# Performance work log

Hardware: AMD Instinct MI355X
Metric: run time of the kernel (lower is better)

## Reference

```python
import jax, jax.numpy as jnp
import numpy as np

N_NODES = 50000
N_EDGES = 500000
D = 128  # in_size == out_size


def setup_inputs() -> dict:
    key = jax.random.key(0)
    ks = jax.random.split(key, 12)
    s = 1.0 / np.sqrt(D)
    feats = jax.random.normal(ks[0], (N_NODES, D), dtype=jnp.float32)
    # per-etype Linear params (torch Linear: y = x @ W.T + b)
    W_chem = jax.random.uniform(ks[1], (D, D), jnp.float32, -s, s)
    b_chem = jax.random.uniform(ks[2], (D,), jnp.float32, -s, s)
    W_elec = jax.random.uniform(ks[3], (D, D), jnp.float32, -s, s)
    b_elec = jax.random.uniform(ks[4], (D,), jnp.float32, -s, s)
    W_out = jax.random.uniform(ks[5], (D, D), jnp.float32, -s, s)
    b_out = jax.random.uniform(ks[6], (D,), jnp.float32, -s, s)
    src_chem = jax.random.randint(ks[7], (N_EDGES,), 0, N_NODES, dtype=jnp.int32)
    dst_chem = jax.random.randint(ks[8], (N_EDGES,), 0, N_NODES, dtype=jnp.int32)
    src_elec = jax.random.randint(ks[9], (N_EDGES,), 0, N_NODES, dtype=jnp.int32)
    dst_elec = jax.random.randint(ks[10], (N_EDGES,), 0, N_NODES, dtype=jnp.int32)
    return {
        "feats": feats,
        "W_chem": W_chem, "b_chem": b_chem,
        "W_elec": W_elec, "b_elec": b_elec,
        "W_out": W_out, "b_out": b_out,
        "src_chem": src_chem, "dst_chem": dst_chem,
        "src_elec": src_elec, "dst_elec": dst_elec,
    }


def reference(feats, W_chem, b_chem, W_elec, b_elec, W_out, b_out,
              src_chem, dst_chem, src_elec, dst_elec):
    n = feats.shape[0]
    # Per-etype linear projection of all node features
    Wh_chem = feats @ W_chem.T + b_chem  # [N, D]
    Wh_elec = feats @ W_elec.T + b_elec  # [N, D]
    # copy_src + sum scatter-aggregation per etype, merged with 'sum'
    h = jax.ops.segment_sum(Wh_chem[src_chem], dst_chem, num_segments=n)
    h = h + jax.ops.segment_sum(Wh_elec[src_elec], dst_elec, num_segments=n)
    # output Linear plus the last-iterated etype's Wh (quirk of original code:
    # 'electrical' is last in etypes order)
    return h @ W_out.T + b_out + Wh_elec
```

## Files before the change

kernel.cpp:

```cpp
#include <hip/hip_runtime.h>

#define D 128
#define PAD 48

typedef __attribute__((ext_vector_type(8))) short bf16x8;
typedef __attribute__((ext_vector_type(4))) float f32x4;

__device__ __forceinline__ unsigned short f2bf(float x) {
    unsigned int u = __float_as_uint(x);
    u += 0x7fffu + ((u >> 16) & 1u);
    return (unsigned short)(u >> 16);
}
__device__ __forceinline__ unsigned int pk2(float lo, float hi) {
    return ((unsigned int)f2bf(hi) << 16) | (unsigned int)f2bf(lo);
}
__device__ __forceinline__ float bf_lo(unsigned int u) { return __uint_as_float(u << 16); }
__device__ __forceinline__ float bf_hi(unsigned int u) { return __uint_as_float(u & 0xffff0000u); }

#define ACC8(U, P, Q)                                   \
        P.x += bf_lo(U.x); P.y += bf_hi(U.x);           \
        P.z += bf_lo(U.y); P.w += bf_hi(U.y);           \
        Q.x += bf_lo(U.z); Q.y += bf_hi(U.z);           \
        Q.z += bf_lo(U.w); Q.w += bf_hi(U.w);

__device__ __forceinline__ void agg_row(const unsigned short* __restrict__ fbf,
                                        const unsigned short* __restrict__ csr,
                                        const int* __restrict__ cnt,
                                        unsigned short* __restrict__ S,
                                        int v, int off) {
    const int deg = min(cnt[v], PAD);
    const unsigned short* row = csr + (size_t)v * PAD;
    float4 a0 = make_float4(0.f,0.f,0.f,0.f), b0 = make_float4(0.f,0.f,0.f,0.f);
    float4 a1 = make_float4(0.f,0.f,0.f,0.f), b1 = make_float4(0.f,0.f,0.f,0.f);
    float4 a2 = make_float4(0.f,0.f,0.f,0.f), b2 = make_float4(0.f,0.f,0.f,0.f);
    float4 a3 = make_float4(0.f,0.f,0.f,0.f), b3 = make_float4(0.f,0.f,0.f,0.f);
    int e = 0;
    for (; e + 4 <= deg; e += 4) {
        int i0 = row[e + 0];
        int i1 = row[e + 1];
        int i2 = row[e + 2];
        int i3 = row[e + 3];
        uint4 u0 = *(const uint4*)(fbf + (size_t)i0 * D + off);
        uint4 u1 = *(const uint4*)(fbf + (size_t)i1 * D + off);
        uint4 u2 = *(const uint4*)(fbf + (size_t)i2 * D + off);
        uint4 u3 = *(const uint4*)(fbf + (size_t)i3 * D + off);
        ACC8(u0, a0, b0) ACC8(u1, a1, b1) ACC8(u2, a2, b2) ACC8(u3, a3, b3)
    }
    for (; e < deg; ++e) {
        int sv = row[e];
        uint4 u = *(const uint4*)(fbf + (size_t)sv * D + off);
        ACC8(u, a0, b0)
    }
    a0.x += a1.x + a2.x + a3.x;  a0.y += a1.y + a2.y + a3.y;
    a0.z += a1.z + a2.z + a3.z;  a0.w += a1.w + a2.w + a3.w;
    b0.x += b1.x + b2.x + b3.x;  b0.y += b1.y + b2.y + b3.y;
    b0.z += b1.z + b2.z + b3.z;  b0.w += b1.w + b2.w + b3.w;
    uint4 o;
    o.x = pk2(a0.x, a0.y); o.y = pk2(a0.z, a0.w);
    o.z = pk2(b0.x, b0.y); o.w = pk2(b0.z, b0.w);
    *(uint4*)(S + (size_t)v * D + off) = o;
}

__global__ __launch_bounds__(256) void wzero(
    const float* __restrict__ Wc, const float* __restrict__ We,
    const float* __restrict__ Wo, const float* __restrict__ b_c,
    const float* __restrict__ b_e, const float* __restrict__ b_o,
    unsigned short* __restrict__ wall, float* __restrict__ bco,
    float* __restrict__ beo, float* __restrict__ bsum,
    int* __restrict__ cnt, int nzero) {
    const int id = blockIdx.x * 256 + threadIdx.x;
    for (int i = id; i < nzero; i += gridDim.x * 256) cnt[i] = 0;
    if (id < 16384) {
        const int j = id >> 7, k = id & 127;
        float s1 = 0.f, s2 = 0.f;
        for (int m = 0; m < 128; ++m) {
            float wo = Wo[j * 128 + m];
            s1 = fmaf(wo, Wc[m * 128 + k], s1);
            s2 = fmaf(wo, We[m * 128 + k], s2);
        }
        wall[j * 128 + k]         = f2bf(s1);
        wall[16384 + j * 128 + k] = f2bf(s2);
        wall[32768 + j * 128 + k] = f2bf(We[j * 128 + k]);
        if (k == 0) {
            float t1 = 0.f, t2 = 0.f;
            for (int m = 0; m < 128; ++m) {
                float wo = Wo[j * 128 + m];
                t1 = fmaf(wo, b_c[m], t1);
                t2 = fmaf(wo, b_e[m], t2);
            }
            bco[j] = t1; beo[j] = t2; bsum[j] = b_o[j] + b_e[j];
        }
    }
}

__global__ __launch_bounds__(256) void fillcv(
    const float4* __restrict__ f, uint4* __restrict__ o, int n8,
    const int* __restrict__ sc, const int* __restrict__ dc,
    int* __restrict__ cnt, unsigned short* __restrict__ csr, int E) {
    int i = blockIdx.x * 256 + threadIdx.x;
    if (i < n8) {
        float4 a = f[2 * i];
        float4 b = f[2 * i + 1];
        o[i] = make_uint4(pk2(a.x, a.y), pk2(a.z, a.w), pk2(b.x, b.y), pk2(b.z, b.w));
    }
    if (i < E) {
        int d = dc[i], s = sc[i];
        int pos = atomicAdd(&cnt[d], 1);
        if (pos < PAD) csr[(size_t)d * PAD + pos] = (unsigned short)s;
    }
}

__global__ __launch_bounds__(256) void fe_ac(
    const unsigned short* __restrict__ fbf,
    const int* __restrict__ se, const int* __restrict__ de,
    int* __restrict__ cnt, unsigned short* __restrict__ csr,
    unsigned short* __restrict__ S,
    int E, int N, int nf, int total) {
    const int bid = blockIdx.x;
    const int f0 = (int)(((long long)bid * nf) / total);
    const int f1 = (int)(((long long)(bid + 1) * nf) / total);
    if (f1 > f0) {
        const int i = f0 * 256 + threadIdx.x;
        if (i < E) {
            int d = de[i] + N, s = se[i];
            int pos = atomicAdd(&cnt[d], 1);
            if (pos < PAD) csr[(size_t)d * PAD + pos] = (unsigned short)s;
        }
    } else {
        const int aidx = bid - f0;
        const int wv  = threadIdx.x >> 6;
        const int ln  = threadIdx.x & 63;
        const int sub = ln >> 4;
        const int l16 = ln & 15;
        const int v = aidx * 16 + wv * 4 + sub;
        if (v < N) agg_row(fbf, csr, cnt, S, v, l16 * 8);
    }
}

__global__ __launch_bounds__(1024) void aggregate_bf(const unsigned short* __restrict__ fbf,
                                                     const unsigned short* __restrict__ csr,
                                                     const int* __restrict__ cnt,
                                                     unsigned short* __restrict__ S,
                                                     int base, int nend) {
    const int wv  = threadIdx.x >> 6;
    const int ln  = threadIdx.x & 63;
    const int sub = ln >> 4;
    const int l16 = ln & 15;
    const int v   = base + blockIdx.x * 64 + wv * 4 + sub;
    if (v < nend) agg_row(fbf, csr, cnt, S, v, l16 * 8);
}

__global__ __launch_bounds__(256, 4) void gemm_direct(
    const unsigned short* __restrict__ S,
    const unsigned short* __restrict__ fbf,
    const unsigned short* __restrict__ wall,
    const float* __restrict__ bco, const float* __restrict__ beo,
    const float* __restrict__ bsum,
    const int* __restrict__ degc, const int* __restrict__ dege,
    float* __restrict__ out, int M) {
    const int t    = threadIdx.x;
    const int r0   = blockIdx.x * 64;
    const int w    = t >> 6;
    const int lane = t & 63;
    const int ln   = lane & 15;
    const int quad = lane >> 4;

    const int r      = r0 + w * 16 + ln;
    const bool valid = (r < M);
    const unsigned short* wB = wall + (size_t)ln * 128 + quad * 8;

    f32x4 acc[8];
#pragma unroll
    for (int g = 0; g < 8; ++g) acc[g] = (f32x4){0.f, 0.f, 0.f, 0.f};

    const bf16x8 azero = {0, 0, 0, 0, 0, 0, 0, 0};

    const unsigned short* ap0 = S + (size_t)r * 128 + quad * 8;
    const unsigned short* ap1 = S + (size_t)(M + r) * 128 + quad * 8;
    const unsigned short* ap2 = fbf + (size_t)r * 128 + quad * 8;

#define PHASE(P, AP)                                                                 \
    {                                                                                \
        _Pragma("unroll") for (int ks = 0; ks < 4; ++ks) {                           \
            bf16x8 a = valid ? *(const bf16x8*)((AP) + ks * 32) : azero;             \
            _Pragma("unroll") for (int g = 0; g < 8; ++g) {                          \
                bf16x8 b = *(const bf16x8*)(wB + (P) * 16384 + g * 2048 + ks * 32);  \
                acc[g] = __builtin_amdgcn_mfma_f32_16x16x32_bf16(a, b, acc[g],       \
                                                                 0, 0, 0);           \
            }                                                                        \
        }                                                                            \
    }

    PHASE(0, ap0)
    PHASE(1, ap1)
    PHASE(2, ap2)
#undef PHASE

    float dcv[4], dev[4];
    int   rrv[4];
#pragma unroll
    for (int rg = 0; rg < 4; ++rg) {
        const int rr = r0 + w * 16 + quad * 4 + rg;
        rrv[rg] = rr;
        dcv[rg] = (rr < M) ? (float)degc[rr] : 0.f;
        dev[rg] = (rr < M) ? (float)dege[rr] : 0.f;
    }
#pragma unroll
    for (int g = 0; g < 8; ++g) {
        const int col = g * 16 + ln;
        const float bc = bco[col], be = beo[col], bs = bsum[col];
#pragma unroll
        for (int rg = 0; rg < 4; ++rg) {
            if (rrv[rg] < M) {
                out[(size_t)rrv[rg] * 128 + col] =
                    acc[g][rg] + bs + dcv[rg] * bc + dev[rg] * be;
            }
        }
    }
}


extern "C" void kernel_launch(void* const* d_in, const int* in_sizes, int n_in,
                              void* d_out, int out_size, void* d_ws, size_t ws_size,
                              hipStream_t stream) {
    const float* feats  = (const float*)d_in[0];
    const float* W_chem = (const float*)d_in[1];
    const float* b_chem = (const float*)d_in[2];
    const float* W_elec = (const float*)d_in[3];
    const float* b_elec = (const float*)d_in[4];
    const float* W_out  = (const float*)d_in[5];
    const float* b_out  = (const float*)d_in[6];
    const int* src_chem = (const int*)d_in[7];
    const int* dst_chem = (const int*)d_in[8];
    const int* src_elec = (const int*)d_in[9];
    const int* dst_elec = (const int*)d_in[10];
    float* out = (float*)d_out;

    const int N = in_sizes[0] / D;
    const int E = in_sizes[7];
    const int N2 = 2 * N;

    unsigned short* fbf  = (unsigned short*)d_ws;
    unsigned short* S    = fbf + (size_t)N * D;
    unsigned short* wall = S + (size_t)N2 * D;
    float* bco  = (float*)(wall + 3 * 16384);
    float* beo  = bco + 128;
    float* bsum = beo + 128;
    int* cnt    = (int*)(bsum + 128);
    unsigned short* csr = (unsigned short*)(cnt + N2);

    const int n8 = N * D / 8;
    const int nf = (E + 255) / 256;
    const int na = (N + 15) / 16;
    const int total = nf + na;

    wzero<<<512, 256, 0, stream>>>(W_chem, W_elec, W_out, b_chem, b_elec, b_out,
                                   wall, bco, beo, bsum, cnt, N2);
    fillcv<<<(n8 + 255) / 256, 256, 0, stream>>>(
        (const float4*)feats, (uint4*)fbf, n8, src_chem, dst_chem, cnt, csr, E);
    fe_ac<<<total, 256, 0, stream>>>(fbf, src_elec, dst_elec, cnt, csr, S,
                                     E, N, nf, total);
    aggregate_bf<<<(N + 63) / 64, 1024, 0, stream>>>(fbf, csr, cnt, S, N, N2);
    gemm_direct<<<(N + 63) / 64, 256, 0, stream>>>(S, fbf, wall, bco, beo, bsum,
                                                   cnt, cnt + N, out, N);
}
```

Baseline: 254.8 us.

## Stage combined weights in swizzled LDS for GEMM and fold weight prep into fill

The output GEMM now uses 1024-thread blocks covering 256 rows. Each block first copies all three bf16 weight matrices (96 KB) into XOR-swizzled shared memory, and the B operands are then read from LDS instead of global/L2. Weight-product preparation moves from a separate kernel into the feature-conversion/CSR-fill kernel, and counter zeroing becomes a small dedicated kernel. The large LDS allocation limits occupancy to about one block per CU, and the weight-prep threads now share work with the conversion kernel's leading blocks.

```diff
diff --git a/kernel.cpp b/kernel.cpp
--- a/kernel.cpp
+++ b/kernel.cpp
@@ -61,17 +61,33 @@
     *(uint4*)(S + (size_t)v * D + off) = o;
 }
 
-__global__ __launch_bounds__(256) void wzero(
+__global__ __launch_bounds__(256) void zerocnt(int* __restrict__ cnt, int n) {
+    const int i = blockIdx.x * 256 + threadIdx.x;
+    if (i < n) cnt[i] = 0;
+}
+
+__global__ __launch_bounds__(256) void fillcv(
+    const float4* __restrict__ f, uint4* __restrict__ o, int n8,
+    const int* __restrict__ sc, const int* __restrict__ dc,
+    int* __restrict__ cnt, unsigned short* __restrict__ csr, int E,
     const float* __restrict__ Wc, const float* __restrict__ We,
     const float* __restrict__ Wo, const float* __restrict__ b_c,
     const float* __restrict__ b_e, const float* __restrict__ b_o,
     unsigned short* __restrict__ wall, float* __restrict__ bco,
-    float* __restrict__ beo, float* __restrict__ bsum,
-    int* __restrict__ cnt, int nzero) {
-    const int id = blockIdx.x * 256 + threadIdx.x;
-    for (int i = id; i < nzero; i += gridDim.x * 256) cnt[i] = 0;
-    if (id < 16384) {
-        const int j = id >> 7, k = id & 127;
+    float* __restrict__ beo, float* __restrict__ bsum) {
+    const int i = blockIdx.x * 256 + threadIdx.x;
+    if (i < n8) {
+        float4 a = f[2 * i];
+        float4 b = f[2 * i + 1];
+        o[i] = make_uint4(pk2(a.x, a.y), pk2(a.z, a.w), pk2(b.x, b.y), pk2(b.z, b.w));
+    }
+    if (i < E) {
+        int d = dc[i], s = sc[i];
+        int pos = atomicAdd(&cnt[d], 1);
+        if (pos < PAD) csr[(size_t)d * PAD + pos] = (unsigned short)s;
+    }
+    if (i < 16384) {
+        const int j = i >> 7, k = i & 127;
         float s1 = 0.f, s2 = 0.f;
         for (int m = 0; m < 128; ++m) {
             float wo = Wo[j * 128 + m];
@@ -90,23 +106,6 @@
             }
             bco[j] = t1; beo[j] = t2; bsum[j] = b_o[j] + b_e[j];
         }
-    }
-}
-
-__global__ __launch_bounds__(256) void fillcv(
-    const float4* __restrict__ f, uint4* __restrict__ o, int n8,
-    const int* __restrict__ sc, const int* __restrict__ dc,
-    int* __restrict__ cnt, unsigned short* __restrict__ csr, int E) {
-    int i = blockIdx.x * 256 + threadIdx.x;
-    if (i < n8) {
-        float4 a = f[2 * i];
-        float4 b = f[2 * i + 1];
-        o[i] = make_uint4(pk2(a.x, a.y), pk2(a.z, a.w), pk2(b.x, b.y), pk2(b.z, b.w));
-    }
-    if (i < E) {
-        int d = dc[i], s = sc[i];
-        int pos = atomicAdd(&cnt[d], 1);
-        if (pos < PAD) csr[(size_t)d * PAD + pos] = (unsigned short)s;
     }
 }
 
@@ -150,7 +149,7 @@
     if (v < nend) agg_row(fbf, csr, cnt, S, v, l16 * 8);
 }
 
-__global__ __launch_bounds__(256, 4) void gemm_direct(
+__global__ __launch_bounds__(1024) void gemm_w3(
     const unsigned short* __restrict__ S,
     const unsigned short* __restrict__ fbf,
     const unsigned short* __restrict__ wall,
@@ -158,42 +157,57 @@
     const float* __restrict__ bsum,
     const int* __restrict__ degc, const int* __restrict__ dege,
     float* __restrict__ out, int M) {
+    extern __shared__ unsigned int Wt[];
+
     const int t    = threadIdx.x;
-    const int r0   = blockIdx.x * 64;
+    const int r0   = blockIdx.x * 256;
     const int w    = t >> 6;
     const int lane = t & 63;
     const int ln   = lane & 15;
     const int quad = lane >> 4;
+    const int lnx  = ln & 7;
+
+#pragma unroll
+    for (int i2 = 0; i2 < 6; ++i2) {
+        int g2 = i2 * 1024 + t;
+        int p  = g2 >> 11;
+        int gg = g2 & 2047;
+        int j  = gg >> 4;
+        int cc = gg & 15;
+        uint4 v = *(const uint4*)(wall + (size_t)p * 16384 + (size_t)j * 128 + cc * 8);
+        *(uint4*)(Wt + p * 8192 + j * 64 + ((cc ^ (j & 7)) << 2)) = v;
+    }
 
     const int r      = r0 + w * 16 + ln;
     const bool valid = (r < M);
-    const unsigned short* wB = wall + (size_t)ln * 128 + quad * 8;
-
-    f32x4 acc[8];
-#pragma unroll
-    for (int g = 0; g < 8; ++g) acc[g] = (f32x4){0.f, 0.f, 0.f, 0.f};
-
     const bf16x8 azero = {0, 0, 0, 0, 0, 0, 0, 0};
-
     const unsigned short* ap0 = S + (size_t)r * 128 + quad * 8;
     const unsigned short* ap1 = S + (size_t)(M + r) * 128 + quad * 8;
     const unsigned short* ap2 = fbf + (size_t)r * 128 + quad * 8;
 
-#define PHASE(P, AP)                                                                 \
+    f32x4 acc[8];
+#pragma unroll
+    for (int g = 0; g < 8; ++g) acc[g] = (f32x4){0.f, 0.f, 0.f, 0.f};
+
+#define PHASE(AP, P)                                                                 \
     {                                                                                \
+        bf16x8 a[4];                                                                 \
+        _Pragma("unroll") for (int ks = 0; ks < 4; ++ks)                             \
+            a[ks] = valid ? *(const bf16x8*)((AP) + ks * 32) : azero;                \
         _Pragma("unroll") for (int ks = 0; ks < 4; ++ks) {                           \
-            bf16x8 a = valid ? *(const bf16x8*)((AP) + ks * 32) : azero;             \
+            const int cx = (((ks * 4 + quad) ^ lnx) << 2);                           \
             _Pragma("unroll") for (int g = 0; g < 8; ++g) {                          \
-                bf16x8 b = *(const bf16x8*)(wB + (P) * 16384 + g * 2048 + ks * 32);  \
-                acc[g] = __builtin_amdgcn_mfma_f32_16x16x32_bf16(a, b, acc[g],       \
+                bf16x8 b = *(const bf16x8*)(Wt + (P) * 8192 + (g * 16 + ln) * 64 + cx); \
+                acc[g] = __builtin_amdgcn_mfma_f32_16x16x32_bf16(a[ks], b, acc[g],   \
                                                                  0, 0, 0);           \
             }                                                                        \
         }                                                                            \
     }
 
-    PHASE(0, ap0)
-    PHASE(1, ap1)
-    PHASE(2, ap2)
+    __syncthreads();
+    PHASE(ap0, 0)
+    PHASE(ap1, 1)
+    PHASE(ap2, 2)
 #undef PHASE
 
     float dcv[4], dev[4];
@@ -252,15 +266,15 @@
     const int n8 = N * D / 8;
     const int nf = (E + 255) / 256;
     const int na = (N + 15) / 16;
-    const int total = nf + na;
-
-    wzero<<<512, 256, 0, stream>>>(W_chem, W_elec, W_out, b_chem, b_elec, b_out,
-                                   wall, bco, beo, bsum, cnt, N2);
+    const int total1 = nf + na;
+
+    zerocnt<<<(N2 + 255) / 256, 256, 0, stream>>>(cnt, N2);
     fillcv<<<(n8 + 255) / 256, 256, 0, stream>>>(
-        (const float4*)feats, (uint4*)fbf, n8, src_chem, dst_chem, cnt, csr, E);
-    fe_ac<<<total, 256, 0, stream>>>(fbf, src_elec, dst_elec, cnt, csr, S,
-                                     E, N, nf, total);
+        (const float4*)feats, (uint4*)fbf, n8, src_chem, dst_chem, cnt, csr, E,
+        W_chem, W_elec, W_out, b_chem, b_elec, b_out, wall, bco, beo, bsum);
+    fe_ac<<<total1, 256, 0, stream>>>(fbf, src_elec, dst_elec, cnt, csr, S,
+                                      E, N, nf, total1);
     aggregate_bf<<<(N + 63) / 64, 1024, 0, stream>>>(fbf, csr, cnt, S, N, N2);
-    gemm_direct<<<(N + 63) / 64, 256, 0, stream>>>(S, fbf, wall, bco, beo, bsum,
-                                                   cnt, cnt + N, out, N);
-}
+    gemm_w3<<<(N + 255) / 256, 1024, 98304, stream>>>(S, fbf, wall, bco, beo,
+                                                      bsum, cnt, cnt + N, out, N);
+}
```

Measured after the change: 224.9 us. 1.13x faster.

## Stage GEMM weights in double-buffered XOR-swizzled LDS with 128-row blocks

Applied to the files above, without the earlier changes.

The final GEMM kernel now copies each 128x128 bf16 weight matrix into shared memory, XOR-swizzled to avoid bank conflicts, and double-buffers the three weight phases so the next phase's global load overlaps the current phase's MFMAs. Blocks grow to 512 threads covering 128 rows, so weight reuse per load doubles. Per-lane global B loads become LDS reads, at the cost of 64KB of LDS per block, which limits occupancy, plus extra barriers.

```diff
diff --git a/kernel.cpp b/kernel.cpp
--- a/kernel.cpp
+++ b/kernel.cpp
@@ -150,7 +150,7 @@
     if (v < nend) agg_row(fbf, csr, cnt, S, v, l16 * 8);
 }
 
-__global__ __launch_bounds__(256, 4) void gemm_direct(
+__global__ __launch_bounds__(512, 4) void gemm_db(
     const unsigned short* __restrict__ S,
     const unsigned short* __restrict__ fbf,
     const unsigned short* __restrict__ wall,
@@ -158,43 +158,74 @@
     const float* __restrict__ bsum,
     const int* __restrict__ degc, const int* __restrict__ dege,
     float* __restrict__ out, int M) {
+    __shared__ unsigned int Wt[2][8192];
+
     const int t    = threadIdx.x;
-    const int r0   = blockIdx.x * 64;
+    const int r0   = blockIdx.x * 128;
     const int w    = t >> 6;
     const int lane = t & 63;
     const int ln   = lane & 15;
     const int quad = lane >> 4;
+    const int lnx  = ln & 7;
 
     const int r      = r0 + w * 16 + ln;
     const bool valid = (r < M);
-    const unsigned short* wB = wall + (size_t)ln * 128 + quad * 8;
-
-    f32x4 acc[8];
-#pragma unroll
-    for (int g = 0; g < 8; ++g) acc[g] = (f32x4){0.f, 0.f, 0.f, 0.f};
-
     const bf16x8 azero = {0, 0, 0, 0, 0, 0, 0, 0};
-
     const unsigned short* ap0 = S + (size_t)r * 128 + quad * 8;
     const unsigned short* ap1 = S + (size_t)(M + r) * 128 + quad * 8;
     const unsigned short* ap2 = fbf + (size_t)r * 128 + quad * 8;
 
-#define PHASE(P, AP)                                                                 \
+    f32x4 acc[8];
+#pragma unroll
+    for (int g = 0; g < 8; ++g) acc[g] = (f32x4){0.f, 0.f, 0.f, 0.f};
+
+    int soff[4], doff[4];
+#pragma unroll
+    for (int i2 = 0; i2 < 4; ++i2) {
+        const int g2 = i2 * 512 + t;
+        const int j  = g2 >> 4;
+        const int cc = g2 & 15;
+        soff[i2] = j * 128 + cc * 8;
+        doff[i2] = j * 64 + ((cc ^ (j & 7)) << 2);
+    }
+    uint4 u[4];
+
+#define LOADW(P)                                                                \
+    _Pragma("unroll") for (int i2 = 0; i2 < 4; ++i2)                            \
+        u[i2] = *(const uint4*)(wall + (size_t)(P) * 16384 + soff[i2]);
+#define WRITEW(BUF)                                                             \
+    _Pragma("unroll") for (int i2 = 0; i2 < 4; ++i2)                            \
+        *(uint4*)(&Wt[BUF][doff[i2]]) = u[i2];
+
+#define PHASE(AP, BUF)                                                               \
     {                                                                                \
+        bf16x8 a[4];                                                                 \
+        _Pragma("unroll") for (int ks = 0; ks < 4; ++ks)                             \
+            a[ks] = valid ? *(const bf16x8*)((AP) + ks * 32) : azero;                \
         _Pragma("unroll") for (int ks = 0; ks < 4; ++ks) {                           \
-            bf16x8 a = valid ? *(const bf16x8*)((AP) + ks * 32) : azero;             \
+            const int cx = (((ks * 4 + quad) ^ lnx) << 2);                           \
             _Pragma("unroll") for (int g = 0; g < 8; ++g) {                          \
-                bf16x8 b = *(const bf16x8*)(wB + (P) * 16384 + g * 2048 + ks * 32);  \
-                acc[g] = __builtin_amdgcn_mfma_f32_16x16x32_bf16(a, b, acc[g],       \
+                bf16x8 b = *(const bf16x8*)(&Wt[BUF][(g * 16 + ln) * 64 + cx]);      \
+                acc[g] = __builtin_amdgcn_mfma_f32_16x16x32_bf16(a[ks], b, acc[g],   \
                                                                  0, 0, 0);           \
             }                                                                        \
         }                                                                            \
     }
 
-    PHASE(0, ap0)
-    PHASE(1, ap1)
-    PHASE(2, ap2)
+    LOADW(0) WRITEW(0)
+    __syncthreads();
+    LOADW(1)
+    PHASE(ap0, 0)
+    WRITEW(1)
+    __syncthreads();
+    LOADW(2)
+    PHASE(ap1, 1)
+    WRITEW(0)
+    __syncthreads();
+    PHASE(ap2, 0)
 #undef PHASE
+#undef WRITEW
+#undef LOADW
 
     float dcv[4], dev[4];
     int   rrv[4];
@@ -252,15 +283,15 @@
     const int n8 = N * D / 8;
     const int nf = (E + 255) / 256;
     const int na = (N + 15) / 16;
-    const int total = nf + na;
+    const int total1 = nf + na;
 
     wzero<<<512, 256, 0, stream>>>(W_chem, W_elec, W_out, b_chem, b_elec, b_out,
                                    wall, bco, beo, bsum, cnt, N2);
     fillcv<<<(n8 + 255) / 256, 256, 0, stream>>>(
         (const float4*)feats, (uint4*)fbf, n8, src_chem, dst_chem, cnt, csr, E);
-    fe_ac<<<total, 256, 0, stream>>>(fbf, src_elec, dst_elec, cnt, csr, S,
-                                     E, N, nf, total);
+    fe_ac<<<total1, 256, 0, stream>>>(fbf, src_elec, dst_elec, cnt, csr, S,
+                                      E, N, nf, total1);
     aggregate_bf<<<(N + 63) / 64, 1024, 0, stream>>>(fbf, csr, cnt, S, N, N2);
-    gemm_direct<<<(N + 63) / 64, 256, 0, stream>>>(S, fbf, wall, bco, beo, bsum,
-                                                   cnt, cnt + N, out, N);
-}
+    gemm_db<<<(N + 127) / 128, 512, 0, stream>>>(S, fbf, wall, bco, beo,
+                                                 bsum, cnt, cnt + N, out, N);
+}
```

Result: faster. 220.8 us (-13.4%).
